# Optimization experiments

Hardware: AMD Instinct MI355X
Metric: run time of the kernel (lower is better)

## Reference

```python
import jax, jax.numpy as jnp
import numpy as np

N_NODES = 100000
BN_EPS = 1e-5


def _cheb_bn_prelu(x, src, dst, w, W, b, a, g, be):
    # ChebConv K=3 with sym normalization, lambda_max=2 => L_hat = -D^-1/2 A D^-1/2
    def lap(v):
        return jax.ops.segment_sum(w[:, None] * v[src], dst, num_segments=N_NODES)
    Tx1 = lap(x)                      # [N, F]
    Tx2 = 2.0 * lap(Tx1) - x
    out = x @ W[0] + Tx1 @ W[1] + Tx2 @ W[2] + b
    out = jnp.where(out > 0, out, a * out)          # PReLU (single param)
    mu = out.mean(0)
    var = out.var(0)                                 # biased, as torch BN
    return (out - mu) / jnp.sqrt(var + BN_EPS) * g + be


def setup_inputs() -> dict:
    key = jax.random.key(0)
    ks = jax.random.split(key, 40)
    N, E, H = N_NODES, 3200000, 64
    inp = {
        'x': jax.random.normal(ks[0], (N, 3), jnp.float32),
        'pos': jax.random.normal(ks[1], (N, 3), jnp.float32),
        'normals': jax.random.normal(ks[2], (N, 3), jnp.float32),
        'edge_index': jax.random.randint(ks[3], (2, E), 0, N, jnp.int64 if jax.config.read('jax_enable_x64') else jnp.int32),
    }
    dims = [(9, H), (H, H), (H, H), (H, H // 2)]
    i = 4
    for m, (fi, fo) in enumerate(dims, start=1):
        s = 1.0 / np.sqrt(fi)
        inp[f'W{m}'] = jax.random.uniform(ks[i], (3, fi, fo), jnp.float32, -s, s); i += 1
        inp[f'b{m}'] = jax.random.uniform(ks[i], (fo,), jnp.float32, -s, s); i += 1
        inp[f'a{m}'] = jnp.full((1,), 0.25, jnp.float32)
        inp[f'g{m}'] = jnp.ones((fo,), jnp.float32)
        inp[f'be{m}'] = jnp.zeros((fo,), jnp.float32)
    hh = H // 2
    for m in range(1, 4):
        s = 1.0 / np.sqrt(hh)
        inp[f'h{m}w'] = jax.random.uniform(ks[i], (hh, hh), jnp.float32, -s, s); i += 1
        inp[f'h{m}b'] = jax.random.uniform(ks[i], (hh,), jnp.float32, -s, s); i += 1
    return inp


def reference(x, pos, normals, edge_index,
              W1, b1, a1, g1, be1, W2, b2, a2, g2, be2,
              W3, b3, a3, g3, be3, W4, b4, a4, g4, be4,
              h1w, h1b, h2w, h2b, h3w, h3b):
    src, dst = edge_index[0], edge_index[1]
    deg = jax.ops.segment_sum(jnp.ones(src.shape[0], x.dtype), src, num_segments=N_NODES)
    dis = jnp.where(deg > 0, jax.lax.rsqrt(jnp.maximum(deg, 1.0)), 0.0)
    w = -dis[src] * dis[dst]                         # scaled Laplacian edge weights
    h = jnp.concatenate([x, pos, normals], axis=1)   # [N, 9]
    h = _cheb_bn_prelu(h, src, dst, w, W1, b1, a1, g1, be1)
    h = _cheb_bn_prelu(h, src, dst, w, W2, b2, a2, g2, be2)
    h = _cheb_bn_prelu(h, src, dst, w, W3, b3, a3, g3, be3)
    h = _cheb_bn_prelu(h, src, dst, w, W4, b4, a4, g4, be4)
    h = jax.nn.relu(h @ h1w + h1b)
    h = jax.nn.relu(h @ h2w + h2b)
    return h @ h3w + h3b                              # [N, 32] logits
```

## Files before the change

kernel.cpp:

```cpp
#include <hip/hip_runtime.h>

constexpr float BN_EPS = 1e-5f;
constexpr int HB = 256;

using short8  = __attribute__((ext_vector_type(8))) short;
using floatx4 = __attribute__((ext_vector_type(4))) float;

__device__ __forceinline__ float bf2f(unsigned short u) {
  return __uint_as_float(((unsigned)u) << 16);
}
__device__ __forceinline__ unsigned short f2bf(float f) {
  union { float f; unsigned u; } v; v.f = f;
  unsigned r = v.u + 0x7FFF + ((v.u >> 16) & 1);
  return (unsigned short)(r >> 16);
}


__global__ void __launch_bounds__(1024) hist_lds_kernel(const int* __restrict__ keys, int E, int slice,
                                                        unsigned* __restrict__ partials, int NW) {
  extern __shared__ unsigned lds[];
  int tid = threadIdx.x, b = blockIdx.x;
  for (int w = tid; w < NW; w += 1024) lds[w] = 0;
  __syncthreads();
  int e0 = b * slice, e1 = e0 + slice; if (e1 > E) e1 = E;
  for (int e = e0 + tid; e < e1; e += 1024) {
    int n = keys[e];
    atomicAdd(&lds[n >> 2], 1u << (8 * (n & 3)));
  }
  __syncthreads();
  unsigned* out = partials + (size_t)b * NW;
  for (int w = tid; w < NW; w += 1024) out[w] = lds[w];
}

__global__ void combine_kernel(unsigned* __restrict__ pA, const unsigned* __restrict__ pB,
                               float* __restrict__ dis, int* __restrict__ cnt, int NW, int N) {
  int w = blockIdx.x * blockDim.x + threadIdx.x;
  if (w >= NW) return;
  unsigned sumA = 0;
  for (int b = 0; b < HB; ++b) sumA += pA[(size_t)b * NW + w];
  unsigned runB = 0;
  for (int b = 0; b < HB; ++b) {
    unsigned v = pB[(size_t)b * NW + w];
    pA[(size_t)b * NW + w] = runB;
    runB += v;
  }
  int n0 = w * 4;
#pragma unroll
  for (int j = 0; j < 4; ++j) {
    int n = n0 + j;
    if (n < N) {
      unsigned da = (sumA >> (8 * j)) & 255u;
      unsigned db = (runB >> (8 * j)) & 255u;
      dis[n] = da > 0 ? rsqrtf((float)da) : 0.f;
      cnt[n] = (int)db;
    }
  }
}

__global__ void scan1_kernel(const int* __restrict__ cnt, int N,
                             int* __restrict__ rowptr, int* __restrict__ bsums) {
  int tid = threadIdx.x, lane = tid & 63, wid = tid >> 6;
  int i = blockIdx.x * 256 + tid;
  int v = (i < N) ? cnt[i] : 0;
  int incl = v;
#pragma unroll
  for (int off = 1; off < 64; off <<= 1) {
    int u = __shfl_up(incl, off);
    if (lane >= off) incl += u;
  }
  __shared__ int wt[4];
  if (lane == 63) wt[wid] = incl;
  __syncthreads();
  int woff = 0;
  for (int w = 0; w < wid; ++w) woff += wt[w];
  if (i < N) rowptr[i] = woff + incl - v;
  if (tid == 255) bsums[blockIdx.x] = woff + incl;
}

__global__ void scan2_kernel(int* __restrict__ bsums, int NB, int* __restrict__ rowptr, int N) {
  int tid = threadIdx.x, lane = tid & 63, wid = tid >> 6;
  int v = (tid < NB) ? bsums[tid] : 0;
  int incl = v;
#pragma unroll
  for (int off = 1; off < 64; off <<= 1) {
    int u = __shfl_up(incl, off);
    if (lane >= off) incl += u;
  }
  __shared__ int wt[16];
  if (lane == 63) wt[wid] = incl;
  __syncthreads();
  int woff = 0;
  for (int w = 0; w < wid; ++w) woff += wt[w];
  if (tid < NB) bsums[tid] = woff + incl - v;
  if (tid == blockDim.x - 1) rowptr[N] = woff + incl;
}

__global__ void scan3_kernel(int* __restrict__ rowptr, const int* __restrict__ bsums, int N) {
  int i = blockIdx.x * 256 + threadIdx.x;
  if (i < N) rowptr[i] += bsums[blockIdx.x];
}

__global__ void __launch_bounds__(1024) scatter2_kernel(
    const int* __restrict__ src, const int* __restrict__ dst, int E, int slice,
    const unsigned* __restrict__ baseTbl, int NW, const int* __restrict__ rowptr,
    const float* __restrict__ dis, int2* __restrict__ pk) {
  extern __shared__ unsigned lds[];
  int tid = threadIdx.x, b = blockIdx.x;
  const unsigned* base = baseTbl + (size_t)b * NW;
  for (int w = tid; w < NW; w += 1024) lds[w] = base[w];
  __syncthreads();
  int e0 = b * slice, e1 = e0 + slice; if (e1 > E) e1 = E;
  for (int e = e0 + tid; e < e1; e += 1024) {
    int s = src[e], d = dst[e];
    unsigned prev = atomicAdd(&lds[d >> 2], 1u << (8 * (d & 3)));
    int p = rowptr[d] + (int)((prev >> (8 * (d & 3))) & 255u);
    pk[p] = make_int2(s, __float_as_int(-dis[s] * dis[d]));
  }
}

__global__ void pack_kernel(const float* __restrict__ x, const float* __restrict__ pos,
                            const float* __restrict__ nrm, ushort* __restrict__ h0c, int N) {
  int idx = blockIdx.x * blockDim.x + threadIdx.x;
  if (idx < N * 64) {
    int n = idx >> 6, c = idx & 63;
    float v = 0.f;
    if (c < 3) v = x[n * 3 + c];
    else if (c < 6) v = pos[n * 3 + c - 3];
    else if (c < 9) v = nrm[n * 3 + c - 6];
    h0c[idx] = f2bf(v);
  }
}


template <bool AFFINE>
__global__ __launch_bounds__(256) void lap64_kernel(
    const ushort4* __restrict__ vb, ushort4* __restrict__ outb,
    const int* __restrict__ rowptr, const int2* __restrict__ pk,
    const float* __restrict__ st, int N) {
  int tid = threadIdx.x, lane = tid & 63, wid = tid >> 6;
  int node = blockIdx.x * 4 + wid;
  if (node >= N) return;
  int g = lane >> 4, q = lane & 15;
  int r0 = rowptr[node], r1 = rowptr[node + 1];
  float4 a = {0.f, 0.f, 0.f, 0.f}, b = {0.f, 0.f, 0.f, 0.f};
  float ws = 0.f, ws2 = 0.f;
  int k = r0 + g;
  for (; k + 12 < r1; k += 16) {
    int2 p0 = pk[k], p1 = pk[k + 4], p2 = pk[k + 8], p3 = pk[k + 12];
    ushort4 u0 = vb[(size_t)p0.x * 16 + q];
    ushort4 u1 = vb[(size_t)p1.x * 16 + q];
    ushort4 u2 = vb[(size_t)p2.x * 16 + q];
    ushort4 u3 = vb[(size_t)p3.x * 16 + q];
    float w0 = __int_as_float(p0.y), w1 = __int_as_float(p1.y);
    float w2 = __int_as_float(p2.y), w3 = __int_as_float(p3.y);
    ws += w0 + w2; ws2 += w1 + w3;
    a.x = fmaf(w0, bf2f(u0.x), a.x); a.y = fmaf(w0, bf2f(u0.y), a.y);
    a.z = fmaf(w0, bf2f(u0.z), a.z); a.w = fmaf(w0, bf2f(u0.w), a.w);
    b.x = fmaf(w1, bf2f(u1.x), b.x); b.y = fmaf(w1, bf2f(u1.y), b.y);
    b.z = fmaf(w1, bf2f(u1.z), b.z); b.w = fmaf(w1, bf2f(u1.w), b.w);
    a.x = fmaf(w2, bf2f(u2.x), a.x); a.y = fmaf(w2, bf2f(u2.y), a.y);
    a.z = fmaf(w2, bf2f(u2.z), a.z); a.w = fmaf(w2, bf2f(u2.w), a.w);
    b.x = fmaf(w3, bf2f(u3.x), b.x); b.y = fmaf(w3, bf2f(u3.y), b.y);
    b.z = fmaf(w3, bf2f(u3.z), b.z); b.w = fmaf(w3, bf2f(u3.w), b.w);
  }
  for (; k < r1; k += 4) {
    int2 p0 = pk[k];
    ushort4 u0 = vb[(size_t)p0.x * 16 + q];
    float w0 = __int_as_float(p0.y);
    ws += w0;
    a.x = fmaf(w0, bf2f(u0.x), a.x); a.y = fmaf(w0, bf2f(u0.y), a.y);
    a.z = fmaf(w0, bf2f(u0.z), a.z); a.w = fmaf(w0, bf2f(u0.w), a.w);
  }
  a.x += b.x; a.y += b.y; a.z += b.z; a.w += b.w; ws += ws2;
  a.x += __shfl_xor(a.x, 16); a.y += __shfl_xor(a.y, 16);
  a.z += __shfl_xor(a.z, 16); a.w += __shfl_xor(a.w, 16);
  ws += __shfl_xor(ws, 16);
  a.x += __shfl_xor(a.x, 32); a.y += __shfl_xor(a.y, 32);
  a.z += __shfl_xor(a.z, 32); a.w += __shfl_xor(a.w, 32);
  ws += __shfl_xor(ws, 32);
  if (g == 0) {
    float4 o = a;
    if (AFFINE) {
      float4 s4 = *(const float4*)(st + q * 4);
      float4 t4 = *(const float4*)(st + 64 + q * 4);
      o.x = fmaf(a.x, s4.x, ws * t4.x);
      o.y = fmaf(a.y, s4.y, ws * t4.y);
      o.z = fmaf(a.z, s4.z, ws * t4.z);
      o.w = fmaf(a.w, s4.w, ws * t4.w);
    }
    ushort4 ub;
    ub.x = f2bf(o.x); ub.y = f2bf(o.y); ub.z = f2bf(o.z); ub.w = f2bf(o.w);
    outb[(size_t)node * 16 + q] = ub;
  }
}


__global__ __launch_bounds__(256) void lap16_kernel(const ushort4* __restrict__ vb,
                                                    ushort4* __restrict__ outb,
                                                    const int* __restrict__ rowptr,
                                                    const int2* __restrict__ pk, int N,
                                                    int inOff, int outOff) {
  int tid = threadIdx.x, lane = tid & 63, wid = tid >> 6;
  int node = (blockIdx.x * 4 + wid) * 4 + (lane >> 4);
  int sub = lane & 15, g = sub >> 2, q = sub & 3;
  float4 acc = {0.f, 0.f, 0.f, 0.f};
  if (node < N) {
    int r0 = rowptr[node], r1 = rowptr[node + 1];
    int k = r0 + g;
    for (; k + 4 < r1; k += 8) {
      int2 pa = pk[k], pb = pk[k + 4];
      ushort4 ua = vb[(size_t)pa.x * 16 + inOff + q];
      ushort4 ub2 = vb[(size_t)pb.x * 16 + inOff + q];
      float wa = __int_as_float(pa.y), wb = __int_as_float(pb.y);
      acc.x = fmaf(wa, bf2f(ua.x), acc.x); acc.y = fmaf(wa, bf2f(ua.y), acc.y);
      acc.z = fmaf(wa, bf2f(ua.z), acc.z); acc.w = fmaf(wa, bf2f(ua.w), acc.w);
      acc.x = fmaf(wb, bf2f(ub2.x), acc.x); acc.y = fmaf(wb, bf2f(ub2.y), acc.y);
      acc.z = fmaf(wb, bf2f(ub2.z), acc.z); acc.w = fmaf(wb, bf2f(ub2.w), acc.w);
    }
    if (k < r1) {
      int2 pr = pk[k];
      float w = __int_as_float(pr.y);
      ushort4 u = vb[(size_t)pr.x * 16 + inOff + q];
      acc.x = fmaf(w, bf2f(u.x), acc.x); acc.y = fmaf(w, bf2f(u.y), acc.y);
      acc.z = fmaf(w, bf2f(u.z), acc.z); acc.w = fmaf(w, bf2f(u.w), acc.w);
    }
  }
  acc.x += __shfl_xor(acc.x, 4); acc.y += __shfl_xor(acc.y, 4);
  acc.z += __shfl_xor(acc.z, 4); acc.w += __shfl_xor(acc.w, 4);
  acc.x += __shfl_xor(acc.x, 8); acc.y += __shfl_xor(acc.y, 8);
  acc.z += __shfl_xor(acc.z, 8); acc.w += __shfl_xor(acc.w, 8);
  if (node < N && g == 0) {
    ushort4 ub;
    ub.x = f2bf(acc.x); ub.y = f2bf(acc.y); ub.z = f2bf(acc.z); ub.w = f2bf(acc.w);
    outb[(size_t)node * 16 + outOff + q] = ub;
  }
}


template <int NMAT, int F_OUT, bool NORMH>
__device__ __forceinline__ void buildW(const float* __restrict__ W, const float* __restrict__ bias,
                                       const float* stPrev,
                                       ushort* __restrict__ fragW, float* __restrict__ biasP,
                                       int f_in_real, int tid, int nth) {
  constexpr int NFRAG = F_OUT / 16;
  constexpr int NKF = NMAT * 2;
  constexpr int TOTF = NKF * NFRAG;
  const int S = f_in_real * F_OUT;
  for (int idx = tid; idx < TOTF * 512; idx += nth) {
    int f = idx >> 9;
    int r = idx & 511;
    int l = r >> 3, j = r & 7;
    int kf = f / NFRAG, nc = f - kf * NFRAG;
    int c = nc * 16 + (l & 15);
    float v = 0.f;
    if (NMAT == 3) {
      int k = (kf & 1) * 32 + (l >> 4) * 8 + j;
      int m = kf >> 1;
      int b = k * F_OUT + c;
      if (m == 0)      { v = W[b] - W[2 * S + b]; if (NORMH) v *= stPrev[k]; }
      else if (m == 1)   v = W[S + b];
      else               v = 2.f * W[2 * S + b];
    } else {
      int kg = kf * 32 + (l >> 4) * 8 + j;
      int sub = kg >> 4, kk = kg & 15;
      if (sub < 3 && kk < f_in_real) {
        int b = kk * F_OUT + c;
        if (sub == 0)      v = W[b] - W[2 * S + b];
        else if (sub == 1) v = W[S + b];
        else               v = 2.f * W[2 * S + b];
      }
    }
    fragW[idx] = f2bf(v);
  }
  if (tid < F_OUT) {
    float acc = bias[tid];
    if (NORMH) {
      for (int k = 0; k < 64; ++k)
        acc += stPrev[64 + k] * (W[k * F_OUT + tid] - W[2 * S + k * F_OUT + tid]);
    }
    biasP[tid] = acc;
  }
}

__global__ void __launch_bounds__(1024) wprep1_kernel(const float* __restrict__ W,
                                                      const float* __restrict__ bias,
                                                      ushort* __restrict__ fragW,
                                                      float* __restrict__ biasP, int finr) {
  buildW<1, 64, false>(W, bias, nullptr, fragW, biasP, finr, threadIdx.x, 1024);
}


template <int NMAT, int F_OUT>
__global__ __launch_bounds__(256) void mmfma_kernel(
    const ushort* __restrict__ A0, const ushort* __restrict__ A1, const ushort* __restrict__ A2,
    ushort* __restrict__ outb,
    const ushort* __restrict__ fragW, const float* __restrict__ biasP,
    const float* __restrict__ aP,
    float* __restrict__ bp, int N, int ntiles) {
  constexpr int NFRAG = F_OUT / 16;
  constexpr int NKF = NMAT * 2;
  constexpr int TOTF = NKF * NFRAG;
  __shared__ float red[4 * 2 * 64];
  int tid = threadIdx.x;
  for (int idx = tid; idx < 512; idx += 256) red[idx] = 0.f;
  __syncthreads();

  const int lane = tid & 63, wid = tid >> 6;
  const int rg = lane >> 4, cl = lane & 15;
  const float alpha = aP[0];

  short8 bfr[TOTF];
#pragma unroll
  for (int f = 0; f < TOTF; ++f)
    bfr[f] = *(const short8*)&fragW[f * 512 + lane * 8];
  float bi[NFRAG];
#pragma unroll
  for (int nc = 0; nc < NFRAG; ++nc) bi[nc] = biasP[nc * 16 + cl];

  float ssum[NFRAG], ssq[NFRAG];
#pragma unroll
  for (int nc = 0; nc < NFRAG; ++nc) { ssum[nc] = 0.f; ssq[nc] = 0.f; }

  for (int tile = blockIdx.x; tile < ntiles; tile += gridDim.x) {
    const int nb = tile * 64 + wid * 16;
    floatx4 acc[NFRAG];
#pragma unroll
    for (int nc = 0; nc < NFRAG; ++nc) acc[nc] = (floatx4){0.f, 0.f, 0.f, 0.f};

#pragma unroll
    for (int kf = 0; kf < NKF; ++kf) {
      const ushort* Ap = (NMAT == 1) ? A0 : (kf < 2 ? A0 : (kf < 4 ? A1 : A2));
      int kc = kf & 1;
      short8 a = *(const short8*)(Ap + (size_t)(nb + cl) * 64 + kc * 32 + rg * 8);
#pragma unroll
      for (int nc = 0; nc < NFRAG; ++nc)
        acc[nc] = __builtin_amdgcn_mfma_f32_16x16x32_bf16(a, bfr[kf * NFRAG + nc], acc[nc], 0, 0, 0);
    }

#pragma unroll
    for (int nc = 0; nc < NFRAG; ++nc) {
      int c = nc * 16 + cl;
#pragma unroll
      for (int r = 0; r < 4; ++r) {
        int node = nb + rg * 4 + r;
        if (node < N) {
          float t = acc[nc][r] + bi[nc];
          t = t > 0.f ? t : alpha * t;
          ssum[nc] += t; ssq[nc] += t * t;
          outb[(size_t)node * 64 + c] = f2bf(t);
        }
      }
    }
  }

#pragma unroll
  for (int nc = 0; nc < NFRAG; ++nc) {
    ssum[nc] += __shfl_xor(ssum[nc], 16); ssum[nc] += __shfl_xor(ssum[nc], 32);
    ssq[nc]  += __shfl_xor(ssq[nc], 16);  ssq[nc]  += __shfl_xor(ssq[nc], 32);
  }
  if (lane < 16) {
#pragma unroll
    for (int nc = 0; nc < NFRAG; ++nc) {
      red[(wid * 2 + 0) * 64 + nc * 16 + lane] = ssum[nc];
      red[(wid * 2 + 1) * 64 + nc * 16 + lane] = ssq[nc];
    }
  }
  __syncthreads();
  if (tid < 128) {
    int col = tid & 63, stat = tid >> 6;
    float tot = red[(0 * 2 + stat) * 64 + col] + red[(1 * 2 + stat) * 64 + col]
              + red[(2 * 2 + stat) * 64 + col] + red[(3 * 2 + stat) * 64 + col];
    bp[(size_t)blockIdx.x * 128 + stat * 64 + col] = tot;
  }
}


template <int NMAT_N, int F_OUT_N, bool BUILD>
__global__ void stats_kernel(const float* __restrict__ bp, int nb,
                             const float* __restrict__ g, const float* __restrict__ be,
                             float* __restrict__ st, int F_OUT, float invN,
                             const float* __restrict__ Wn, const float* __restrict__ bn,
                             ushort* __restrict__ fragWn, float* __restrict__ biasPn, int finrN) {
  __shared__ float red[1024];
  __shared__ float stSh[128];
  int tid = threadIdx.x;
  int t = tid & 127, c = tid >> 7;
  float s = 0.f;
  for (int w = c; w < nb; w += 8) s += bp[(size_t)w * 128 + t];
  red[tid] = s;
  __syncthreads();
  if (tid < 128) {
    float tot = 0.f;
    for (int cc = 0; cc < 8; ++cc) tot += red[cc * 128 + tid];
    red[tid] = tot;
  }
  __syncthreads();
  if (tid < F_OUT) {
    float sum = red[tid], sq = red[64 + tid];
    float mu = sum * invN;
    float var = sq * invN - mu * mu;
    float sc = g[tid] * rsqrtf(var + BN_EPS);
    st[tid] = sc;        stSh[tid] = sc;
    st[64 + tid] = be[tid] - mu * sc;
    stSh[64 + tid] = be[tid] - mu * sc;
  }
  if (BUILD) {
    __syncthreads();
    buildW<NMAT_N, F_OUT_N, true>(Wn, bn, stSh, fragWn, biasPn, finrN, tid, 1024);
  }
}


__global__ __launch_bounds__(256) void mlp_kernel(const ushort* __restrict__ hb,
    const float* __restrict__ st,
    const float* __restrict__ w1, const float* __restrict__ b1,
    const float* __restrict__ w2, const float* __restrict__ b2,
    const float* __restrict__ w3, const float* __restrict__ b3,
    float* __restrict__ out, int N, int ntiles) {
  __shared__ float Wl[3][1024];
  __shared__ float Bl[3][32];
  __shared__ float S4[32], T4[32];
  __shared__ float act[2][128][36];
  int tid = threadIdx.x;
  for (int idx = tid; idx < 1024; idx += 256) {
    Wl[0][idx] = w1[idx];
    Wl[1][idx] = w2[idx];
    Wl[2][idx] = w3[idx];
  }
  if (tid < 32) {
    Bl[0][tid] = b1[tid]; Bl[1][tid] = b2[tid]; Bl[2][tid] = b3[tid];
    S4[tid] = st[tid]; T4[tid] = st[64 + tid];
  }
  __syncthreads();

  const int cg = tid & 7, ng = tid >> 3;
  const int c0 = cg * 4;
  const int nl = ng * 4;

  for (int tile = blockIdx.x; tile < ntiles; tile += gridDim.x) {
    const int node0 = tile * 128 + nl;
    float acc[4][4];

#pragma unroll
    for (int j = 0; j < 4; ++j)
#pragma unroll
      for (int c = 0; c < 4; ++c) acc[j][c] = 0.f;
#pragma unroll
    for (int kb = 0; kb < 8; ++kb) {
      float ar[4][4];
#pragma unroll
      for (int j = 0; j < 4; ++j) {
        int node = node0 + j;
        if (node < N) {
          ushort4 u = *(const ushort4*)(hb + (size_t)node * 64 + kb * 4);
          ar[j][0] = fmaf(bf2f(u.x), S4[kb * 4 + 0], T4[kb * 4 + 0]);
          ar[j][1] = fmaf(bf2f(u.y), S4[kb * 4 + 1], T4[kb * 4 + 1]);
          ar[j][2] = fmaf(bf2f(u.z), S4[kb * 4 + 2], T4[kb * 4 + 2]);
          ar[j][3] = fmaf(bf2f(u.w), S4[kb * 4 + 3], T4[kb * 4 + 3]);
        } else {
          ar[j][0] = ar[j][1] = ar[j][2] = ar[j][3] = 0.f;
        }
      }
#pragma unroll
      for (int kk = 0; kk < 4; ++kk) {
        float br[4];
        *(float4*)br = *(const float4*)(&Wl[0][(kb * 4 + kk) * 32 + c0]);
#pragma unroll
        for (int j = 0; j < 4; ++j)
#pragma unroll
          for (int c = 0; c < 4; ++c)
            acc[j][c] = fmaf(ar[j][kk], br[c], acc[j][c]);
      }
    }
#pragma unroll
    for (int j = 0; j < 4; ++j) {
      float v[4];
#pragma unroll
      for (int c = 0; c < 4; ++c) v[c] = fmaxf(acc[j][c] + Bl[0][c0 + c], 0.f);
      *(float4*)(&act[0][nl + j][c0]) = *(float4*)v;
    }
    __syncthreads();

#pragma unroll
    for (int j = 0; j < 4; ++j)
#pragma unroll
      for (int c = 0; c < 4; ++c) acc[j][c] = 0.f;
#pragma unroll
    for (int kb = 0; kb < 8; ++kb) {
      float ar[4][4];
#pragma unroll
      for (int j = 0; j < 4; ++j)
        *(float4*)ar[j] = *(const float4*)(&act[0][nl + j][kb * 4]);
#pragma unroll
      for (int kk = 0; kk < 4; ++kk) {
        float br[4];
        *(float4*)br = *(const float4*)(&Wl[1][(kb * 4 + kk) * 32 + c0]);
#pragma unroll
        for (int j = 0; j < 4; ++j)
#pragma unroll
          for (int c = 0; c < 4; ++c)
            acc[j][c] = fmaf(ar[j][kk], br[c], acc[j][c]);
      }
    }
#pragma unroll
    for (int j = 0; j < 4; ++j) {
      float v[4];
#pragma unroll
      for (int c = 0; c < 4; ++c) v[c] = fmaxf(acc[j][c] + Bl[1][c0 + c], 0.f);
      *(float4*)(&act[1][nl + j][c0]) = *(float4*)v;
    }
    __syncthreads();

#pragma unroll
    for (int j = 0; j < 4; ++j)
#pragma unroll
      for (int c = 0; c < 4; ++c) acc[j][c] = 0.f;
#pragma unroll
    for (int kb = 0; kb < 8; ++kb) {
      float ar[4][4];
#pragma unroll
      for (int j = 0; j < 4; ++j)
        *(float4*)ar[j] = *(const float4*)(&act[1][nl + j][kb * 4]);
#pragma unroll
      for (int kk = 0; kk < 4; ++kk) {
        float br[4];
        *(float4*)br = *(const float4*)(&Wl[2][(kb * 4 + kk) * 32 + c0]);
#pragma unroll
        for (int j = 0; j < 4; ++j)
#pragma unroll
          for (int c = 0; c < 4; ++c)
            acc[j][c] = fmaf(ar[j][kk], br[c], acc[j][c]);
      }
    }
#pragma unroll
    for (int j = 0; j < 4; ++j) {
      int node = node0 + j;
      if (node < N) {
        float v[4];
#pragma unroll
        for (int c = 0; c < 4; ++c) v[c] = acc[j][c] + Bl[2][c0 + c];
        *(float4*)(out + (size_t)node * 32 + c0) = *(float4*)v;
      }
    }
    __syncthreads();
  }
}


extern "C" void kernel_launch(void* const* d_in, const int* in_sizes, int n_in,
                              void* d_out, int out_size, void* d_ws, size_t ws_size,
                              hipStream_t stream) {
  const float* x   = (const float*)d_in[0];
  const float* pos = (const float*)d_in[1];
  const float* nrm = (const float*)d_in[2];
  const int*   ei  = (const int*)d_in[3];
  const float* W1p = (const float*)d_in[4];
  const float* b1p = (const float*)d_in[5];
  const float* a1p = (const float*)d_in[6];
  const float* g1p = (const float*)d_in[7];
  const float* be1p= (const float*)d_in[8];
  const float* W2p = (const float*)d_in[9];
  const float* b2p = (const float*)d_in[10];
  const float* a2p = (const float*)d_in[11];
  const float* g2p = (const float*)d_in[12];
  const float* be2p= (const float*)d_in[13];
  const float* W3p = (const float*)d_in[14];
  const float* b3p = (const float*)d_in[15];
  const float* a3p = (const float*)d_in[16];
  const float* g3p = (const float*)d_in[17];
  const float* be3p= (const float*)d_in[18];
  const float* W4p = (const float*)d_in[19];
  const float* b4p = (const float*)d_in[20];
  const float* a4p = (const float*)d_in[21];
  const float* g4p = (const float*)d_in[22];
  const float* be4p= (const float*)d_in[23];
  const float* h1w = (const float*)d_in[24];
  const float* h1b = (const float*)d_in[25];
  const float* h2w = (const float*)d_in[26];
  const float* h2b = (const float*)d_in[27];
  const float* h3w = (const float*)d_in[28];
  const float* h3b = (const float*)d_in[29];

  const int N = in_sizes[0] / 3;
  const int E = in_sizes[3] / 2;
  const int* src = ei;
  const int* dst = ei + E;

  const int NW = (N + 3) / 4;
  const size_t ldsBytes = (size_t)NW * 4;
  const int slice = (E + HB - 1) / HB;

  char* p = (char*)d_ws;
  auto alloc = [&](size_t bytes) -> void* {
    void* r = (void*)p;
    p += (bytes + 255) & ~(size_t)255;
    return r;
  };
  float*    dis      = (float*)   alloc((size_t)N * 4);
  int*      rowptr   = (int*)     alloc((size_t)(N + 1) * 4);
  int*      cnt      = (int*)     alloc((size_t)N * 4);
  int*      bsums    = (int*)     alloc(4096 * 4);
  unsigned* partialsA= (unsigned*)alloc((size_t)HB * NW * 4);
  unsigned* partialsB= (unsigned*)alloc((size_t)HB * NW * 4);
  int2*     pk       = (int2*)partialsB;
  ushort*   bufHb    = (ushort*)  alloc((size_t)N * 64 * 2);
  ushort*   bufT1b   = (ushort*)  alloc((size_t)N * 64 * 2);
  ushort*   bufT2b   = (ushort*)  alloc((size_t)N * 64 * 2);
  ushort*   bufC16   = (ushort*)  alloc((size_t)N * 64 * 2);
  const int MMB = 782;
  float*    bp       = (float*)   alloc((size_t)MMB * 128 * 4);
  float*    stats    = (float*)   alloc(512 * 4);
  ushort*   fragW    = (ushort*)  alloc(24 * 512 * 2);
  float*    biasP    = (float*)   alloc(64 * 4);
  float* st1 = stats, *st2 = stats + 128, *st3 = stats + 256, *st4 = stats + 384;

  int gN = (N + 255) / 256;
  hist_lds_kernel<<<HB, 1024, ldsBytes, stream>>>(src, E, slice, partialsA, NW);
  hist_lds_kernel<<<HB, 1024, ldsBytes, stream>>>(dst, E, slice, partialsB, NW);
  combine_kernel<<<(NW + 255) / 256, 256, 0, stream>>>(partialsA, partialsB, dis, cnt, NW, N);
  scan1_kernel<<<gN, 256, 0, stream>>>(cnt, N, rowptr, bsums);
  scan2_kernel<<<1, 1024, 0, stream>>>(bsums, gN, rowptr, N);
  scan3_kernel<<<gN, 256, 0, stream>>>(rowptr, bsums, N);
  scatter2_kernel<<<HB, 1024, ldsBytes, stream>>>(src, dst, E, slice, partialsA, NW, rowptr, dis, pk);
  pack_kernel<<<(N * 64 + 255) / 256, 256, 0, stream>>>(x, pos, nrm, bufC16, N);
  wprep1_kernel<<<1, 1024, 0, stream>>>(W1p, b1p, fragW, biasP, 9);

  const float invN = 1.f / (float)N;
  int g64 = (N + 3) / 4, g16 = (N + 15) / 16;
  const int ntiles = (N + 63) / 64;
  const int ntilesM = (N + 127) / 128;

  lap16_kernel<<<g16, 256, 0, stream>>>((const ushort4*)bufC16, (ushort4*)bufC16, rowptr, pk, N, 0, 4);
  lap16_kernel<<<g16, 256, 0, stream>>>((const ushort4*)bufC16, (ushort4*)bufC16, rowptr, pk, N, 4, 8);
  mmfma_kernel<1, 64><<<MMB, 256, 0, stream>>>(bufC16, nullptr, nullptr, bufHb,
      fragW, biasP, a1p, bp, N, ntiles);
  stats_kernel<3, 64, true><<<1, 1024, 0, stream>>>(bp, MMB, g1p, be1p, st1, 64, invN,
      W2p, b2p, fragW, biasP, 64);

  lap64_kernel<true><<<g64, 256, 0, stream>>>((const ushort4*)bufHb, (ushort4*)bufT1b,
      rowptr, pk, st1, N);
  lap64_kernel<false><<<g64, 256, 0, stream>>>((const ushort4*)bufT1b, (ushort4*)bufT2b,
      rowptr, pk, nullptr, N);
  mmfma_kernel<3, 64><<<MMB, 256, 0, stream>>>(bufHb, bufT1b, bufT2b, bufHb,
      fragW, biasP, a2p, bp, N, ntiles);
  stats_kernel<3, 64, true><<<1, 1024, 0, stream>>>(bp, MMB, g2p, be2p, st2, 64, invN,
      W3p, b3p, fragW, biasP, 64);

  lap64_kernel<true><<<g64, 256, 0, stream>>>((const ushort4*)bufHb, (ushort4*)bufT1b,
      rowptr, pk, st2, N);
  lap64_kernel<false><<<g64, 256, 0, stream>>>((const ushort4*)bufT1b, (ushort4*)bufT2b,
      rowptr, pk, nullptr, N);
  mmfma_kernel<3, 64><<<MMB, 256, 0, stream>>>(bufHb, bufT1b, bufT2b, bufHb,
      fragW, biasP, a3p, bp, N, ntiles);
  stats_kernel<3, 32, true><<<1, 1024, 0, stream>>>(bp, MMB, g3p, be3p, st3, 64, invN,
      W4p, b4p, fragW, biasP, 64);

  lap64_kernel<true><<<g64, 256, 0, stream>>>((const ushort4*)bufHb, (ushort4*)bufT1b,
      rowptr, pk, st3, N);
  lap64_kernel<false><<<g64, 256, 0, stream>>>((const ushort4*)bufT1b, (ushort4*)bufT2b,
      rowptr, pk, nullptr, N);
  mmfma_kernel<3, 32><<<MMB, 256, 0, stream>>>(bufHb, bufT1b, bufT2b, bufHb,
      fragW, biasP, a4p, bp, N, ntiles);
  stats_kernel<3, 64, false><<<1, 1024, 0, stream>>>(bp, MMB, g4p, be4p, st4, 32, invN,
      nullptr, nullptr, nullptr, nullptr, 0);

  mlp_kernel<<<ntilesM, 256, 0, stream>>>(bufHb, st4, h1w, h1b, h2w, h2b, h3w, h3b,
      (float*)d_out, N, ntilesM);
}
```

Before: 851.7 us.

## Store only source ids in CSR and recompute edge weights from dis on the fly

The scatter step now writes only the sorted source index per edge instead of an (src, weight) int2 pair, which halves the CSR edge stream. The Laplacian kernels rebuild each weight as -dis[src]*dis[node] with an extra gather into the small dis array. The first layer's 9-feature input, T1 and T2 move from one 64-wide buffer into three separate 16-wide buffers, so the layer-1 gathers and the pack kernel touch less memory. The MFMA kernel reads these split buffers through a zero buffer for the padding slots. The cost is one extra random 4-byte load per edge, which should mostly hit in cache.

Result: no change. 856.0 us (+0.5%).

```diff
diff --git a/kernel.cpp b/kernel.cpp
--- a/kernel.cpp
+++ b/kernel.cpp
@@ -103,7 +103,7 @@
 __global__ void __launch_bounds__(1024) scatter2_kernel(
     const int* __restrict__ src, const int* __restrict__ dst, int E, int slice,
     const unsigned* __restrict__ baseTbl, int NW, const int* __restrict__ rowptr,
-    const float* __restrict__ dis, int2* __restrict__ pk) {
+    int* __restrict__ srcS) {
   extern __shared__ unsigned lds[];
   int tid = threadIdx.x, b = blockIdx.x;
   const unsigned* base = baseTbl + (size_t)b * NW;
@@ -114,20 +114,20 @@
     int s = src[e], d = dst[e];
     unsigned prev = atomicAdd(&lds[d >> 2], 1u << (8 * (d & 3)));
     int p = rowptr[d] + (int)((prev >> (8 * (d & 3))) & 255u);
-    pk[p] = make_int2(s, __float_as_int(-dis[s] * dis[d]));
+    srcS[p] = s;
   }
 }
 
 __global__ void pack_kernel(const float* __restrict__ x, const float* __restrict__ pos,
-                            const float* __restrict__ nrm, ushort* __restrict__ h0c, int N) {
+                            const float* __restrict__ nrm, ushort* __restrict__ h0p, int N) {
   int idx = blockIdx.x * blockDim.x + threadIdx.x;
-  if (idx < N * 64) {
-    int n = idx >> 6, c = idx & 63;
+  if (idx < N * 16) {
+    int n = idx >> 4, c = idx & 15;
     float v = 0.f;
     if (c < 3) v = x[n * 3 + c];
     else if (c < 6) v = pos[n * 3 + c - 3];
     else if (c < 9) v = nrm[n * 3 + c - 6];
-    h0c[idx] = f2bf(v);
+    h0p[idx] = f2bf(v);
   }
 }
 
@@ -135,24 +135,25 @@
 template <bool AFFINE>
 __global__ __launch_bounds__(256) void lap64_kernel(
     const ushort4* __restrict__ vb, ushort4* __restrict__ outb,
-    const int* __restrict__ rowptr, const int2* __restrict__ pk,
-    const float* __restrict__ st, int N) {
+    const int* __restrict__ rowptr, const int* __restrict__ srcS,
+    const float* __restrict__ dis, const float* __restrict__ st, int N) {
   int tid = threadIdx.x, lane = tid & 63, wid = tid >> 6;
   int node = blockIdx.x * 4 + wid;
   if (node >= N) return;
   int g = lane >> 4, q = lane & 15;
+  float disd = -dis[node];
   int r0 = rowptr[node], r1 = rowptr[node + 1];
   float4 a = {0.f, 0.f, 0.f, 0.f}, b = {0.f, 0.f, 0.f, 0.f};
   float ws = 0.f, ws2 = 0.f;
   int k = r0 + g;
   for (; k + 12 < r1; k += 16) {
-    int2 p0 = pk[k], p1 = pk[k + 4], p2 = pk[k + 8], p3 = pk[k + 12];
-    ushort4 u0 = vb[(size_t)p0.x * 16 + q];
-    ushort4 u1 = vb[(size_t)p1.x * 16 + q];
-    ushort4 u2 = vb[(size_t)p2.x * 16 + q];
-    ushort4 u3 = vb[(size_t)p3.x * 16 + q];
-    float w0 = __int_as_float(p0.y), w1 = __int_as_float(p1.y);
-    float w2 = __int_as_float(p2.y), w3 = __int_as_float(p3.y);
+    int s0 = srcS[k], s1 = srcS[k + 4], s2 = srcS[k + 8], s3 = srcS[k + 12];
+    float d0 = dis[s0], d1 = dis[s1], d2 = dis[s2], d3 = dis[s3];
+    ushort4 u0 = vb[(size_t)s0 * 16 + q];
+    ushort4 u1 = vb[(size_t)s1 * 16 + q];
+    ushort4 u2 = vb[(size_t)s2 * 16 + q];
+    ushort4 u3 = vb[(size_t)s3 * 16 + q];
+    float w0 = d0 * disd, w1 = d1 * disd, w2 = d2 * disd, w3 = d3 * disd;
     ws += w0 + w2; ws2 += w1 + w3;
     a.x = fmaf(w0, bf2f(u0.x), a.x); a.y = fmaf(w0, bf2f(u0.y), a.y);
     a.z = fmaf(w0, bf2f(u0.z), a.z); a.w = fmaf(w0, bf2f(u0.w), a.w);
@@ -164,9 +165,9 @@
     b.z = fmaf(w3, bf2f(u3.z), b.z); b.w = fmaf(w3, bf2f(u3.w), b.w);
   }
   for (; k < r1; k += 4) {
-    int2 p0 = pk[k];
-    ushort4 u0 = vb[(size_t)p0.x * 16 + q];
-    float w0 = __int_as_float(p0.y);
+    int s0 = srcS[k];
+    float w0 = dis[s0] * disd;
+    ushort4 u0 = vb[(size_t)s0 * 16 + q];
     ws += w0;
     a.x = fmaf(w0, bf2f(u0.x), a.x); a.y = fmaf(w0, bf2f(u0.y), a.y);
     a.z = fmaf(w0, bf2f(u0.z), a.z); a.w = fmaf(w0, bf2f(u0.w), a.w);
@@ -198,29 +199,30 @@
 __global__ __launch_bounds__(256) void lap16_kernel(const ushort4* __restrict__ vb,
                                                     ushort4* __restrict__ outb,
                                                     const int* __restrict__ rowptr,
-                                                    const int2* __restrict__ pk, int N,
-                                                    int inOff, int outOff) {
+                                                    const int* __restrict__ srcS,
+                                                    const float* __restrict__ dis, int N) {
   int tid = threadIdx.x, lane = tid & 63, wid = tid >> 6;
   int node = (blockIdx.x * 4 + wid) * 4 + (lane >> 4);
   int sub = lane & 15, g = sub >> 2, q = sub & 3;
   float4 acc = {0.f, 0.f, 0.f, 0.f};
   if (node < N) {
+    float disd = -dis[node];
     int r0 = rowptr[node], r1 = rowptr[node + 1];
     int k = r0 + g;
     for (; k + 4 < r1; k += 8) {
-      int2 pa = pk[k], pb = pk[k + 4];
-      ushort4 ua = vb[(size_t)pa.x * 16 + inOff + q];
-      ushort4 ub2 = vb[(size_t)pb.x * 16 + inOff + q];
-      float wa = __int_as_float(pa.y), wb = __int_as_float(pb.y);
+      int sa = srcS[k], sb = srcS[k + 4];
+      float wa = dis[sa] * disd, wb = dis[sb] * disd;
+      ushort4 ua = vb[(size_t)sa * 4 + q];
+      ushort4 ub2 = vb[(size_t)sb * 4 + q];
       acc.x = fmaf(wa, bf2f(ua.x), acc.x); acc.y = fmaf(wa, bf2f(ua.y), acc.y);
       acc.z = fmaf(wa, bf2f(ua.z), acc.z); acc.w = fmaf(wa, bf2f(ua.w), acc.w);
       acc.x = fmaf(wb, bf2f(ub2.x), acc.x); acc.y = fmaf(wb, bf2f(ub2.y), acc.y);
       acc.z = fmaf(wb, bf2f(ub2.z), acc.z); acc.w = fmaf(wb, bf2f(ub2.w), acc.w);
     }
     if (k < r1) {
-      int2 pr = pk[k];
-      float w = __int_as_float(pr.y);
-      ushort4 u = vb[(size_t)pr.x * 16 + inOff + q];
+      int s = srcS[k];
+      float w = dis[s] * disd;
+      ushort4 u = vb[(size_t)s * 4 + q];
       acc.x = fmaf(w, bf2f(u.x), acc.x); acc.y = fmaf(w, bf2f(u.y), acc.y);
       acc.z = fmaf(w, bf2f(u.z), acc.z); acc.w = fmaf(w, bf2f(u.w), acc.w);
     }
@@ -232,7 +234,7 @@
   if (node < N && g == 0) {
     ushort4 ub;
     ub.x = f2bf(acc.x); ub.y = f2bf(acc.y); ub.z = f2bf(acc.z); ub.w = f2bf(acc.w);
-    outb[(size_t)node * 16 + outOff + q] = ub;
+    outb[(size_t)node * 4 + q] = ub;
   }
 }
 
@@ -293,6 +295,7 @@
 template <int NMAT, int F_OUT>
 __global__ __launch_bounds__(256) void mmfma_kernel(
     const ushort* __restrict__ A0, const ushort* __restrict__ A1, const ushort* __restrict__ A2,
+    const ushort* __restrict__ Az,
     ushort* __restrict__ outb,
     const ushort* __restrict__ fragW, const float* __restrict__ biasP,
     const float* __restrict__ aP,
@@ -329,9 +332,17 @@
 
 #pragma unroll
     for (int kf = 0; kf < NKF; ++kf) {
-      const ushort* Ap = (NMAT == 1) ? A0 : (kf < 2 ? A0 : (kf < 4 ? A1 : A2));
-      int kc = kf & 1;
-      short8 a = *(const short8*)(Ap + (size_t)(nb + cl) * 64 + kc * 32 + rg * 8);
+      short8 a;
+      if (NMAT == 3) {
+        const ushort* Ap = (kf < 2 ? A0 : (kf < 4 ? A1 : A2));
+        a = *(const short8*)(Ap + (size_t)(nb + cl) * 64 + (kf & 1) * 32 + rg * 8);
+      } else {
+        int k0 = kf * 32 + rg * 8;
+        int sb = k0 >> 4;
+        const ushort* Ap = sb == 0 ? A0 : (sb == 1 ? A1 : (sb == 2 ? A2 : Az));
+        size_t off = (sb == 3) ? 0 : ((size_t)(nb + cl) * 16 + (k0 & 15));
+        a = *(const short8*)(Ap + off);
+      }
 #pragma unroll
       for (int nc = 0; nc < NFRAG; ++nc)
         acc[nc] = __builtin_amdgcn_mfma_f32_16x16x32_bf16(a, bfr[kf * NFRAG + nc], acc[nc], 0, 0, 0);
@@ -602,11 +613,14 @@
   int*      bsums    = (int*)     alloc(4096 * 4);
   unsigned* partialsA= (unsigned*)alloc((size_t)HB * NW * 4);
   unsigned* partialsB= (unsigned*)alloc((size_t)HB * NW * 4);
-  int2*     pk       = (int2*)partialsB;
+  int*      srcS     = (int*)partialsB;
   ushort*   bufHb    = (ushort*)  alloc((size_t)N * 64 * 2);
   ushort*   bufT1b   = (ushort*)  alloc((size_t)N * 64 * 2);
   ushort*   bufT2b   = (ushort*)  alloc((size_t)N * 64 * 2);
-  ushort*   bufC16   = (ushort*)  alloc((size_t)N * 64 * 2);
+  ushort*   h16p     = (ushort*)  alloc((size_t)N * 16 * 2);
+  ushort*   t1p      = (ushort*)  alloc((size_t)N * 16 * 2);
+  ushort*   t2p      = (ushort*)  alloc((size_t)N * 16 * 2);
+  ushort*   zerob    = (ushort*)  alloc(64);
   const int MMB = 782;
   float*    bp       = (float*)   alloc((size_t)MMB * 128 * 4);
   float*    stats    = (float*)   alloc(512 * 4);
@@ -615,14 +629,15 @@
   float* st1 = stats, *st2 = stats + 128, *st3 = stats + 256, *st4 = stats + 384;
 
   int gN = (N + 255) / 256;
+  hipMemsetAsync(zerob, 0, 64, stream);
   hist_lds_kernel<<<HB, 1024, ldsBytes, stream>>>(src, E, slice, partialsA, NW);
   hist_lds_kernel<<<HB, 1024, ldsBytes, stream>>>(dst, E, slice, partialsB, NW);
   combine_kernel<<<(NW + 255) / 256, 256, 0, stream>>>(partialsA, partialsB, dis, cnt, NW, N);
   scan1_kernel<<<gN, 256, 0, stream>>>(cnt, N, rowptr, bsums);
   scan2_kernel<<<1, 1024, 0, stream>>>(bsums, gN, rowptr, N);
   scan3_kernel<<<gN, 256, 0, stream>>>(rowptr, bsums, N);
-  scatter2_kernel<<<HB, 1024, ldsBytes, stream>>>(src, dst, E, slice, partialsA, NW, rowptr, dis, pk);
-  pack_kernel<<<(N * 64 + 255) / 256, 256, 0, stream>>>(x, pos, nrm, bufC16, N);
+  scatter2_kernel<<<HB, 1024, ldsBytes, stream>>>(src, dst, E, slice, partialsA, NW, rowptr, srcS);
+  pack_kernel<<<(N * 16 + 255) / 256, 256, 0, stream>>>(x, pos, nrm, h16p, N);
   wprep1_kernel<<<1, 1024, 0, stream>>>(W1p, b1p, fragW, biasP, 9);
 
   const float invN = 1.f / (float)N;
@@ -630,36 +645,36 @@
   const int ntiles = (N + 63) / 64;
   const int ntilesM = (N + 127) / 128;
 
-  lap16_kernel<<<g16, 256, 0, stream>>>((const ushort4*)bufC16, (ushort4*)bufC16, rowptr, pk, N, 0, 4);
-  lap16_kernel<<<g16, 256, 0, stream>>>((const ushort4*)bufC16, (ushort4*)bufC16, rowptr, pk, N, 4, 8);
-  mmfma_kernel<1, 64><<<MMB, 256, 0, stream>>>(bufC16, nullptr, nullptr, bufHb,
+  lap16_kernel<<<g16, 256, 0, stream>>>((const ushort4*)h16p, (ushort4*)t1p, rowptr, srcS, dis, N);
+  lap16_kernel<<<g16, 256, 0, stream>>>((const ushort4*)t1p, (ushort4*)t2p, rowptr, srcS, dis, N);
+  mmfma_kernel<1, 64><<<MMB, 256, 0, stream>>>(h16p, t1p, t2p, zerob, bufHb,
       fragW, biasP, a1p, bp, N, ntiles);
   stats_kernel<3, 64, true><<<1, 1024, 0, stream>>>(bp, MMB, g1p, be1p, st1, 64, invN,
       W2p, b2p, fragW, biasP, 64);
 
   lap64_kernel<true><<<g64, 256, 0, stream>>>((const ushort4*)bufHb, (ushort4*)bufT1b,
-      rowptr, pk, st1, N);
+      rowptr, srcS, dis, st1, N);
   lap64_kernel<false><<<g64, 256, 0, stream>>>((const ushort4*)bufT1b, (ushort4*)bufT2b,
-      rowptr, pk, nullptr, N);
-  mmfma_kernel<3, 64><<<MMB, 256, 0, stream>>>(bufHb, bufT1b, bufT2b, bufHb,
+      rowptr, srcS, dis, nullptr, N);
+  mmfma_kernel<3, 64><<<MMB, 256, 0, stream>>>(bufHb, bufT1b, bufT2b, nullptr, bufHb,
       fragW, biasP, a2p, bp, N, ntiles);
   stats_kernel<3, 64, true><<<1, 1024, 0, stream>>>(bp, MMB, g2p, be2p, st2, 64, invN,
       W3p, b3p, fragW, biasP, 64);
 
   lap64_kernel<true><<<g64, 256, 0, stream>>>((const ushort4*)bufHb, (ushort4*)bufT1b,
-      rowptr, pk, st2, N);
+      rowptr, srcS, dis, st2, N);
   lap64_kernel<false><<<g64, 256, 0, stream>>>((const ushort4*)bufT1b, (ushort4*)bufT2b,
-      rowptr, pk, nullptr, N);
-  mmfma_kernel<3, 64><<<MMB, 256, 0, stream>>>(bufHb, bufT1b, bufT2b, bufHb,
+      rowptr, srcS, dis, nullptr, N);
+  mmfma_kernel<3, 64><<<MMB, 256, 0, stream>>>(bufHb, bufT1b, bufT2b, nullptr, bufHb,
       fragW, biasP, a3p, bp, N, ntiles);
   stats_kernel<3, 32, true><<<1, 1024, 0, stream>>>(bp, MMB, g3p, be3p, st3, 64, invN,
       W4p, b4p, fragW, biasP, 64);
 
   lap64_kernel<true><<<g64, 256, 0, stream>>>((const ushort4*)bufHb, (ushort4*)bufT1b,
-      rowptr, pk, st3, N);
+      rowptr, srcS, dis, st3, N);
   lap64_kernel<false><<<g64, 256, 0, stream>>>((const ushort4*)bufT1b, (ushort4*)bufT2b,
-      rowptr, pk, nullptr, N);
-  mmfma_kernel<3, 32><<<MMB, 256, 0, stream>>>(bufHb, bufT1b, bufT2b, bufHb,
+      rowptr, srcS, dis, nullptr, N);
+  mmfma_kernel<3, 32><<<MMB, 256, 0, stream>>>(bufHb, bufT1b, bufT2b, nullptr, bufHb,
       fragW, biasP, a4p, bp, N, ntiles);
   stats_kernel<3, 64, false><<<1, 1024, 0, stream>>>(bp, MMB, g4p, be4p, st4, 32, invN,
       nullptr, nullptr, nullptr, nullptr, 0);
```
